# Performance work log

Measured on AMD Instinct MI355X. Metric: run time of the kernel, lower is better.

The kernel has to match this reference:

```python
import jax, jax.numpy as jnp
import numpy as np

IN_FEATURES = 512
NUM_KNOTS = 64
XMIN = -3.0
XMAX = 3.0


def setup_inputs() -> dict:
    key = jax.random.key(0)
    kx, kc = jax.random.split(key)
    x = jax.random.normal(kx, (65536, IN_FEATURES), dtype=jnp.float32)
    coeffs = jax.random.normal(kc, (IN_FEATURES, NUM_KNOTS), dtype=jnp.float32) * 0.01
    return {"x": x, "coeffs": coeffs}


def reference(x, coeffs):
    # x: (B, F); coeffs: (F, K). Piecewise-linear spline per feature, summed over features.
    K = coeffs.shape[1]
    t = (x - XMIN) / (XMAX - XMIN) * (K - 1)          # (B, F)
    t0 = jnp.clip(jnp.floor(t).astype(jnp.int32), 0, K - 2)
    w1 = t - t0.astype(t.dtype)
    w0 = 1.0 - w1
    feat_idx = jnp.arange(coeffs.shape[0])[None, :]    # (1, F) broadcast with (B, F) indices
    c0 = coeffs[feat_idx, t0]                          # (B, F) gather
    c1 = coeffs[feat_idx, t0 + 1]
    return jnp.sum(w0 * c0 + w1 * c1, axis=1)          # (B,)
```

## Files before the change

kernel.cpp:

```cpp
#include <hip/hip_runtime.h>
#include <stdint.h>


#define ROWS_PER_BLOCK 128

__device__ __forceinline__ uint32_t bf16_rne(float v) {
    uint32_t u = __float_as_uint(v);
    return (u + 0x7fffu + ((u >> 16) & 1u)) >> 16;
}

__global__ __launch_bounds__(1024, 4)
void spline_kernel(const float* __restrict__ x,
                   const float* __restrict__ coeffs,
                   float* __restrict__ out)
{
    __shared__ uint32_t T[256 * 64];

    const int tid  = threadIdx.x;
    const int lane = tid & 63;
    const int w    = tid >> 6;
    const long rowBase = (long)blockIdx.x * ROWS_PER_BLOCK;
    const float lf   = (float)lane;
    const float tadd = 31.5f + lf;
    const float hi   = lf + 62.0f;

    float accR[8] = {0.f, 0.f, 0.f, 0.f, 0.f, 0.f, 0.f, 0.f};

    #pragma unroll
    for (int c = 0; c < 2; ++c) {
        __syncthreads();
        #pragma unroll
        for (int it = 0; it < 16; ++it) {
            const int idx = it * 1024 + tid;
            const int fl  = idx >> 6;
            const int k   = idx & 63;
            const int gi  = c * 16384 + idx;
            const float c0 = coeffs[gi];
            const float c1 = coeffs[gi + (k < 63 ? 1 : 0)];
            const int kp  = (k + (fl >> 2)) & 63;
            T[(idx & ~63) | kp] = (bf16_rne(c0) << 16) | bf16_rne(c1 - c0);
        }
        __syncthreads();

        const float* xb = x + (rowBase + w * 8) * 512 + c * 256 + lane * 4;
        #pragma unroll 2
        for (int r = 0; r < 8; ++r) {
            const float4 v = *reinterpret_cast<const float4*>(xb + r * 512);
            float a = 0.f;
            #pragma unroll
            for (int q = 0; q < 4; ++q) {
                const float xv  = (q == 0) ? v.x : (q == 1) ? v.y : (q == 2) ? v.z : v.w;
                const float tt  = xv * 10.5f + tadd;
                const float t0f = fminf(fmaxf(floorf(tt), lf), hi);
                const uint32_t g = T[(lane << 8) + (q << 6) + (((int)t0f) & 63)];
                a += __uint_as_float(g & 0xffff0000u)
                   + (tt - t0f) * __uint_as_float(g << 16);
            }
            accR[r] += a;
        }
    }

    float stash = 0.f;
    #pragma unroll
    for (int r = 0; r < 8; ++r) {
        float s = accR[r];
        #pragma unroll
        for (int m = 1; m < 64; m <<= 1)
            s += __shfl_xor(s, m, 64);
        if (lane == r) stash = s;
    }
    if (lane < 8) out[rowBase + w * 8 + lane] = stash;
}

extern "C" void kernel_launch(void* const* d_in, const int* in_sizes, int n_in,
                              void* d_out, int out_size, void* d_ws, size_t ws_size,
                              hipStream_t stream) {
    const float* x      = (const float*)d_in[0];
    const float* coeffs = (const float*)d_in[1];
    float* out = (float*)d_out;
    (void)in_sizes; (void)n_in; (void)out_size; (void)d_ws; (void)ws_size;

    dim3 grid(65536 / ROWS_PER_BLOCK);
    dim3 block(1024);
    spline_kernel<<<grid, block, 0, stream>>>(x, coeffs, out);
}
```

Measured before the change: 36.68 us.

## Split features across block pairs with atomic accumulation and prefetched row loads

Each block now builds the LDS coefficient table for only one half of the features, so it runs a single table build and sync instead of two. Twice as many blocks handle 256 rows each and combine their partial sums with atomicAdd into an output zeroed by a memset. Rows are software-prefetched two ahead, the table is built from vectorised float4 coefficient loads using a shuffle for the neighbour value, and clamping uses fmed3. The extra memset launch, the atomics and the higher launch-bounds occupancy target add register pressure and launch overhead in exchange.

```diff
diff --git a/kernel.cpp b/kernel.cpp
--- a/kernel.cpp
+++ b/kernel.cpp
@@ -2,14 +2,19 @@
 #include <stdint.h>
 
 
-#define ROWS_PER_BLOCK 128
+#define ROWS 256
+
+typedef float f32x4 __attribute__((ext_vector_type(4)));
 
 __device__ __forceinline__ uint32_t bf16_rne(float v) {
     uint32_t u = __float_as_uint(v);
     return (u + 0x7fffu + ((u >> 16) & 1u)) >> 16;
 }
+__device__ __forceinline__ uint32_t pack2(float c0, float dc) {
+    return (bf16_rne(c0) << 16) | bf16_rne(dc);
+}
 
-__global__ __launch_bounds__(1024, 4)
+__global__ __launch_bounds__(1024, 8)
 void spline_kernel(const float* __restrict__ x,
                    const float* __restrict__ coeffs,
                    float* __restrict__ out)
@@ -19,57 +24,59 @@
     const int tid  = threadIdx.x;
     const int lane = tid & 63;
     const int w    = tid >> 6;
-    const long rowBase = (long)blockIdx.x * ROWS_PER_BLOCK;
+    const int half = blockIdx.x & 1;
+    const long rowBase = (long)(blockIdx.x >> 1) * ROWS;
+    const int  fbase   = half * 256;
+
+    const float* xw = x + (rowBase + w * 16) * 512 + fbase + lane * 4;
+
+    f32x4 pva = *reinterpret_cast<const f32x4*>(xw);
+    f32x4 pvb = *reinterpret_cast<const f32x4*>(xw + 512);
+
+    #pragma unroll
+    for (int it = 0; it < 4; ++it) {
+        const int g  = it * 1024 + tid;
+        const int fl = g >> 4;
+        const int j  = g & 15;
+        const f32x4 c4 = *reinterpret_cast<const f32x4*>(coeffs + (fbase + fl) * 64 + j * 4);
+        const float nxt = __shfl(c4.x, (lane + 1) & 63, 64);
+        const int scr = fl >> 2;
+        uint32_t* Tf = &T[fl * 64];
+        Tf[(j * 4 + 0 + scr) & 63] = pack2(c4.x, c4.y - c4.x);
+        Tf[(j * 4 + 1 + scr) & 63] = pack2(c4.y, c4.z - c4.y);
+        Tf[(j * 4 + 2 + scr) & 63] = pack2(c4.z, c4.w - c4.z);
+        Tf[(j * 4 + 3 + scr) & 63] = pack2(c4.w, nxt - c4.w);
+    }
+    __syncthreads();
+
     const float lf   = (float)lane;
     const float tadd = 31.5f + lf;
     const float hi   = lf + 62.0f;
 
-    float accR[8] = {0.f, 0.f, 0.f, 0.f, 0.f, 0.f, 0.f, 0.f};
-
-    #pragma unroll
-    for (int c = 0; c < 2; ++c) {
-        __syncthreads();
-        #pragma unroll
-        for (int it = 0; it < 16; ++it) {
-            const int idx = it * 1024 + tid;
-            const int fl  = idx >> 6;
-            const int k   = idx & 63;
-            const int gi  = c * 16384 + idx;
-            const float c0 = coeffs[gi];
-            const float c1 = coeffs[gi + (k < 63 ? 1 : 0)];
-            const int kp  = (k + (fl >> 2)) & 63;
-            T[(idx & ~63) | kp] = (bf16_rne(c0) << 16) | bf16_rne(c1 - c0);
-        }
-        __syncthreads();
-
-        const float* xb = x + (rowBase + w * 8) * 512 + c * 256 + lane * 4;
-        #pragma unroll 2
-        for (int r = 0; r < 8; ++r) {
-            const float4 v = *reinterpret_cast<const float4*>(xb + r * 512);
-            float a = 0.f;
-            #pragma unroll
-            for (int q = 0; q < 4; ++q) {
-                const float xv  = (q == 0) ? v.x : (q == 1) ? v.y : (q == 2) ? v.z : v.w;
-                const float tt  = xv * 10.5f + tadd;
-                const float t0f = fminf(fmaxf(floorf(tt), lf), hi);
-                const uint32_t g = T[(lane << 8) + (q << 6) + (((int)t0f) & 63)];
-                a += __uint_as_float(g & 0xffff0000u)
-                   + (tt - t0f) * __uint_as_float(g << 16);
-            }
-            accR[r] += a;
-        }
-    }
-
     float stash = 0.f;
     #pragma unroll
-    for (int r = 0; r < 8; ++r) {
-        float s = accR[r];
+    for (int r = 0; r < 16; ++r) {
+        const f32x4 v = (r & 1) ? pvb : pva;
+        if (r < 14) {
+            if (r & 1) pvb = *reinterpret_cast<const f32x4*>(xw + (r + 2) * 512);
+            else       pva = *reinterpret_cast<const f32x4*>(xw + (r + 2) * 512);
+        }
+        float a = 0.f;
+        #pragma unroll
+        for (int q = 0; q < 4; ++q) {
+            const float tt  = __builtin_fmaf(v[q], 10.5f, tadd);
+            const float t0f = __builtin_amdgcn_fmed3f(floorf(tt), lf, hi);
+            const uint32_t g = T[(lane << 8) + (q << 6) + (((int)t0f) & 63)];
+            a += __uint_as_float(g & 0xffff0000u)
+               + (tt - t0f) * __uint_as_float(g << 16);
+        }
         #pragma unroll
         for (int m = 1; m < 64; m <<= 1)
-            s += __shfl_xor(s, m, 64);
-        if (lane == r) stash = s;
+            a += __shfl_xor(a, m, 64);
+        if (lane == r) stash = a;
     }
-    if (lane < 8) out[rowBase + w * 8 + lane] = stash;
+    if (lane < 16)
+        atomicAdd(&out[rowBase + w * 16 + lane], stash);
 }
 
 extern "C" void kernel_launch(void* const* d_in, const int* in_sizes, int n_in,
@@ -78,9 +85,10 @@
     const float* x      = (const float*)d_in[0];
     const float* coeffs = (const float*)d_in[1];
     float* out = (float*)d_out;
-    (void)in_sizes; (void)n_in; (void)out_size; (void)d_ws; (void)ws_size;
+    (void)in_sizes; (void)n_in; (void)d_ws; (void)ws_size;
 
-    dim3 grid(65536 / ROWS_PER_BLOCK);
+    hipMemsetAsync(out, 0, (size_t)out_size * sizeof(float), stream);
+    dim3 grid((65536 / ROWS) * 2);
     dim3 block(1024);
     spline_kernel<<<grid, block, 0, stream>>>(x, coeffs, out);
 }
```

Result: slower. 38.57 us (+5.1%).
